# Kernel tuning notes

Measured on AMD Instinct MI355X. Metric: run time of the kernel, lower is better.

The kernel has to match this reference:

```python
import jax, jax.numpy as jnp
import numpy as np

K = 3  # dynamic filter kernel size
EPS = 1e-10


def _filter_norm_spatial(s, std_param):
    # s: (B, K*K, H, W); normalize over filter-tap dim (unbiased std, as torch)
    s = s - s.mean(axis=1, keepdims=True)
    s = s / (s.std(axis=1, keepdims=True, ddof=1) + EPS)
    return s * std_param[None, :, None, None]


def _filter_norm_channel(cf, std_param, B, C):
    # cf: (B, C*K*K); normalize over the K*K taps of each channel
    cf = cf.reshape(B, C, K * K)
    cf = cf - cf.mean(axis=2, keepdims=True)
    cf = cf / (cf.std(axis=2, keepdims=True, ddof=1) + EPS)
    cf = cf.reshape(B, C * K * K) * std_param[None, :]
    return cf.reshape(B, C, K * K)


def _ddf_pack(x, sw, sb, sstd, cw1, cb1, cw2, cb2, cstd):
    B, C, H, W = x.shape
    # spatial branch: 1x1 conv -> per-pixel K*K spatial filter
    s = jnp.einsum('bchw,oc->bohw', x, sw) + sb[None, :, None, None]
    s = _filter_norm_spatial(s, sstd)                      # (B, 9, H, W)
    # channel branch: GAP -> SE MLP -> per-channel K*K filter
    g = x.mean(axis=(2, 3))                                # (B, C)
    h = jax.nn.relu(g @ cw1.T + cb1)                       # (B, mid)
    cf = h @ cw2.T + cb2                                   # (B, C*9)
    cf = _filter_norm_channel(cf, cstd, B, C)              # (B, C, 9)
    # apply decoupled dynamic filter: w[b,c,uv,h,w] = cf[b,c,uv] * s[b,uv,h,w]
    pad = K // 2
    xp = jnp.pad(x, ((0, 0), (0, 0), (pad, pad), (pad, pad)))
    # patches: (B, C, 9, H, W) -- the 9 shifted views (unfold)
    patches = jnp.stack([xp[:, :, i:i + H, j:j + W]
                         for i in range(K) for j in range(K)], axis=2)
    return jnp.einsum('bckhw,bck,bkhw->bchw', patches, cf, s)


def setup_inputs() -> dict:
    key = jax.random.key(0)
    ks = jax.random.split(key, 20)
    nf, mid = 64, 12
    std_scale = np.sqrt(2.0) / K  # calculate_gain('relu') / kernel_size
    d = {'x': jax.random.normal(ks[0], (4, nf, 256, 256), jnp.float32)}
    i = 1
    for p in ('1', '2'):
        d['sw' + p] = jax.random.normal(ks[i], (K * K, nf), jnp.float32) * 0.1; i += 1
        d['sb' + p] = jax.random.normal(ks[i], (K * K,), jnp.float32) * 0.1; i += 1
        d['sstd' + p] = jax.random.normal(ks[i], (K * K,), jnp.float32) * std_scale; i += 1
        d['cw1_' + p] = jax.random.normal(ks[i], (mid, nf), jnp.float32) * 0.1; i += 1
        d['cb1_' + p] = jax.random.normal(ks[i], (mid,), jnp.float32) * 0.1; i += 1
        d['cw2_' + p] = jax.random.normal(ks[i], (nf * K * K, mid), jnp.float32) * 0.1; i += 1
        d['cb2_' + p] = jax.random.normal(ks[i], (nf * K * K,), jnp.float32) * 0.1; i += 1
        d['cstd' + p] = jax.random.normal(ks[i], (nf * K * K,), jnp.float32) * std_scale; i += 1
    return d


def reference(x, sw1, sb1, sstd1, cw1_1, cb1_1, cw2_1, cb2_1, cstd1,
              sw2, sb2, sstd2, cw1_2, cb1_2, cw2_2, cb2_2, cstd2):
    out = _ddf_pack(x, sw1, sb1, sstd1, cw1_1, cb1_1, cw2_1, cb2_1, cstd1)
    out = jax.nn.relu(out)
    out = _ddf_pack(out, sw2, sb2, sstd2, cw1_2, cb1_2, cw2_2, cb2_2, cstd2)
    return x + out
```

## Files before the change

### kernel.cpp

```cpp
#include <hip/hip_runtime.h>

#define B_ 4
#define C_ 64
#define H_ 256
#define W_ 256
#define HW_ (H_*W_)
#define MID_ 12
#define NPB_ 64

__device__ __forceinline__ float wave_reduce64(float v) {
#pragma unroll
    for (int off = 32; off; off >>= 1) v += __shfl_xor(v, off, 64);
    return v;
}

__global__ __launch_bounds__(256, 1) void prep_kernel(const float* __restrict__ x,
    const float* __restrict__ sw, const float* __restrict__ sb,
    const float* __restrict__ sstd, float* __restrict__ sarr, float* __restrict__ gp) {
    const int lane = threadIdx.x & 63, wv = threadIdx.x >> 6;
    const int row = blockIdx.x * 4 + wv;
    const int b = blockIdx.y;
    const int pix = row * W_ + lane * 4;
    __shared__ float lg[4][C_];

    float4 st[9];
#pragma unroll
    for (int t = 0; t < 9; ++t) { float v = sb[t]; st[t] = make_float4(v, v, v, v); }

    const float* xb = x + (size_t)b * C_ * HW_ + pix;
    float4 vA[4], vB[4];
#pragma unroll
    for (int i = 0; i < 4; ++i) vA[i] = *(const float4*)(xb + (size_t)i * HW_);

#define PREP_COMP(BUF, C0) do {                                               \
        _Pragma("unroll")                                                     \
        for (int i_ = 0; i_ < 4; ++i_) {                                      \
            const int c_ = (C0) + i_;                                         \
            float4 v_ = BUF[i_];                                              \
            _Pragma("unroll")                                                 \
            for (int t_ = 0; t_ < 9; ++t_) {                                  \
                const float wt_ = sw[t_ * C_ + c_];                           \
                st[t_].x = fmaf(v_.x, wt_, st[t_].x);                         \
                st[t_].y = fmaf(v_.y, wt_, st[t_].y);                         \
                st[t_].z = fmaf(v_.z, wt_, st[t_].z);                         \
                st[t_].w = fmaf(v_.w, wt_, st[t_].w);                         \
            }                                                                 \
            float g_ = wave_reduce64(((v_.x + v_.y) + (v_.z + v_.w)));        \
            if (lane == 0) lg[wv][c_] = g_;                                   \
        }                                                                     \
    } while (0)

    for (int k = 0; k < C_; k += 8) {
#pragma unroll
        for (int i = 0; i < 4; ++i) vB[i] = *(const float4*)(xb + (size_t)(k + 4 + i) * HW_);
        PREP_COMP(vA, k);
        if (k + 8 < C_) {
#pragma unroll
            for (int i = 0; i < 4; ++i) vA[i] = *(const float4*)(xb + (size_t)(k + 8 + i) * HW_);
        }
        PREP_COMP(vB, k + 4);
    }
#undef PREP_COMP

    {
        float4 mean = make_float4(0, 0, 0, 0);
#pragma unroll
        for (int t = 0; t < 9; ++t) {
            mean.x += st[t].x; mean.y += st[t].y; mean.z += st[t].z; mean.w += st[t].w;
        }
        mean.x *= (1.f/9.f); mean.y *= (1.f/9.f); mean.z *= (1.f/9.f); mean.w *= (1.f/9.f);
        float4 var = make_float4(0, 0, 0, 0);
#pragma unroll
        for (int t = 0; t < 9; ++t) {
            float dx = st[t].x - mean.x, dy = st[t].y - mean.y;
            float dz = st[t].z - mean.z, dw = st[t].w - mean.w;
            var.x = fmaf(dx, dx, var.x); var.y = fmaf(dy, dy, var.y);
            var.z = fmaf(dz, dz, var.z); var.w = fmaf(dw, dw, var.w);
        }
        float ix = 1.f / (sqrtf(var.x * (1.f/8.f)) + 1e-10f);
        float iy = 1.f / (sqrtf(var.y * (1.f/8.f)) + 1e-10f);
        float iz = 1.f / (sqrtf(var.z * (1.f/8.f)) + 1e-10f);
        float iw = 1.f / (sqrtf(var.w * (1.f/8.f)) + 1e-10f);
        float* sp = sarr + ((size_t)b * 9) * HW_ + pix;
#pragma unroll
        for (int t = 0; t < 9; ++t) {
            float sd = sstd[t];
            *(float4*)(sp + (size_t)t * HW_) = make_float4(
                (st[t].x - mean.x) * ix * sd, (st[t].y - mean.y) * iy * sd,
                (st[t].z - mean.z) * iz * sd, (st[t].w - mean.w) * iw * sd);
        }
    }
    __syncthreads();
    if (threadIdx.x < C_) {
        int c = threadIdx.x;
        float s4 = lg[0][c] + lg[1][c] + lg[2][c] + lg[3][c];
        gp[((size_t)b * C_ + c) * NPB_ + blockIdx.x] = s4;
    }
}

__global__ __launch_bounds__(256) void cfk(const float* __restrict__ gp,
    const float* __restrict__ cw1, const float* __restrict__ cb1,
    const float* __restrict__ cw2, const float* __restrict__ cb2,
    const float* __restrict__ cstd, float* __restrict__ cf) {
    const int tid = threadIdx.x;
    const int b = tid >> 6, c = tid & 63;
    __shared__ float gsm[B_][C_];
    __shared__ float hsm[B_][MID_];
    {
        const float4* p4 = (const float4*)(gp + ((size_t)b * C_ + c) * NPB_);
        float s = 0.f;
#pragma unroll
        for (int i = 0; i < NPB_ / 4; ++i) { float4 v = p4[i]; s += (v.x + v.y) + (v.z + v.w); }
        gsm[b][c] = s * (1.f / HW_);
    }
    __syncthreads();
    if (tid < B_ * MID_) {
        int b2 = tid / MID_, m = tid % MID_;
        float a = cb1[m];
        for (int cc = 0; cc < C_; ++cc) a = fmaf(gsm[b2][cc], cw1[m * C_ + cc], a);
        hsm[b2][m] = fmaxf(a, 0.f);
    }
    __syncthreads();
    float v[9];
    float mean = 0.f;
#pragma unroll
    for (int t = 0; t < 9; ++t) {
        int o = c * 9 + t;
        float a = cb2[o];
#pragma unroll
        for (int m = 0; m < MID_; ++m) a = fmaf(hsm[b][m], cw2[o * MID_ + m], a);
        v[t] = a;
        mean += a;
    }
    mean *= (1.f / 9.f);
    float var = 0.f;
#pragma unroll
    for (int t = 0; t < 9; ++t) { float d = v[t] - mean; var += d * d; }
    float inv = 1.f / (sqrtf(var * (1.f / 8.f)) + 1e-10f);
    float* o12 = cf + ((size_t)b * C_ + c) * 12;
#pragma unroll
    for (int t = 0; t < 9; ++t) o12[t] = (v[t] - mean) * inv * cstd[c * 9 + t];
    o12[9] = 0.f; o12[10] = 0.f; o12[11] = 0.f;
}

template<bool PASS1>
__global__ __launch_bounds__(256, 1) void apply_kernel(const float* __restrict__ in,
    const float* __restrict__ sarr, const float* __restrict__ cf,
    const float* __restrict__ swn, const float* __restrict__ sbn,
    const float* __restrict__ sstdn, const float* __restrict__ resid,
    float* __restrict__ out, float* __restrict__ snext, float* __restrict__ gpn) {
    const int lane = threadIdx.x & 63, wv = threadIdx.x >> 6;
    const int row = blockIdx.x * 4 + wv;
    const int b = blockIdx.y;
    const int c0 = PASS1 ? 0 : (blockIdx.z * 32);
    const int NCH = PASS1 ? 64 : 32;
    const int pix = row * W_ + lane * 4;
    __shared__ float lg[4][C_];

    const bool rup = row > 0, rdn = row < H_ - 1;
    const int offUp = rup ? -W_ : 0;
    const int offDn = rdn ? W_ : 0;
    const float fup = rup ? 1.f : 0.f;
    const float fdn = rdn ? 1.f : 0.f;

    float4 s0t[9];
    {
        const float* sp = sarr + ((size_t)b * 9) * HW_ + pix;
#pragma unroll
        for (int t = 0; t < 9; ++t) s0t[t] = *(const float4*)(sp + (size_t)t * HW_);
#pragma unroll
        for (int t = 0; t < 3; ++t) {
            s0t[t].x *= fup; s0t[t].y *= fup; s0t[t].z *= fup; s0t[t].w *= fup;
            s0t[t + 6].x *= fdn; s0t[t + 6].y *= fdn; s0t[t + 6].z *= fdn; s0t[t + 6].w *= fdn;
        }
        if (lane == 0)  { s0t[0].x = 0.f; s0t[3].x = 0.f; s0t[6].x = 0.f; }
        if (lane == 63) { s0t[2].w = 0.f; s0t[5].w = 0.f; s0t[8].w = 0.f; }
    }

    float4 nt[9];
    if (PASS1) {
#pragma unroll
        for (int t = 0; t < 9; ++t) { float v = sbn[t]; nt[t] = make_float4(v, v, v, v); }
    }

    const float* inb = in + (size_t)b * C_ * HW_ + pix;
    const float* cfb = cf + ((size_t)b * C_) * 12;
    const float* rb  = PASS1 ? nullptr : (resid + (size_t)b * C_ * HW_ + pix);
    float* outp = out + (size_t)b * C_ * HW_ + pix;

    float4 bufA[4][3], bufB[4][3], rA[4], rB[4];

#define LOADB(BUF, RV, CH0) do {                                              \
        _Pragma("unroll")                                                     \
        for (int i_ = 0; i_ < 4; ++i_) {                                      \
            const float* p_ = inb + (size_t)((CH0) + i_) * HW_;               \
            BUF[i_][0] = *(const float4*)(p_ + offUp);                        \
            BUF[i_][1] = *(const float4*)(p_);                                \
            BUF[i_][2] = *(const float4*)(p_ + offDn);                        \
            if (!PASS1) RV[i_] = *(const float4*)(rb + (size_t)((CH0) + i_) * HW_); \
        }                                                                     \
    } while (0)

#define COMPB(BUF, RV, CH0) do {                                              \
        _Pragma("unroll")                                                     \
        for (int i_ = 0; i_ < 4; ++i_) {                                      \
            const int ch_ = (CH0) + i_;                                       \
            const float* cfc_ = cfb + (size_t)ch_ * 12;                       \
            float4 acc_ = make_float4(0.f, 0.f, 0.f, 0.f);                    \
            _Pragma("unroll")                                                 \
            for (int dr_ = 0; dr_ < 3; ++dr_) {                               \
                float4 v_ = BUF[i_][dr_];                                     \
                float w0_ = __shfl_up(v_.w, 1, 64);                           \
                float w5_ = __shfl_down(v_.x, 1, 64);                         \
                const float w_[6] = {w0_, v_.x, v_.y, v_.z, v_.w, w5_};       \
                _Pragma("unroll")                                             \
                for (int dc_ = 0; dc_ < 3; ++dc_) {                           \
                    const int t_ = dr_ * 3 + dc_;                             \
                    const float cft_ = cfc_[t_];                              \
                    acc_.x = fmaf(w_[dc_ + 0] * s0t[t_].x, cft_, acc_.x);     \
                    acc_.y = fmaf(w_[dc_ + 1] * s0t[t_].y, cft_, acc_.y);     \
                    acc_.z = fmaf(w_[dc_ + 2] * s0t[t_].z, cft_, acc_.z);     \
                    acc_.w = fmaf(w_[dc_ + 3] * s0t[t_].w, cft_, acc_.w);     \
                }                                                             \
            }                                                                 \
            float4 o_;                                                        \
            if (PASS1) {                                                      \
                o_.x = fmaxf(acc_.x, 0.f); o_.y = fmaxf(acc_.y, 0.f);         \
                o_.z = fmaxf(acc_.z, 0.f); o_.w = fmaxf(acc_.w, 0.f);         \
                _Pragma("unroll")                                             \
                for (int t_ = 0; t_ < 9; ++t_) {                              \
                    const float wt_ = swn[t_ * C_ + ch_];                     \
                    nt[t_].x = fmaf(o_.x, wt_, nt[t_].x);                     \
                    nt[t_].y = fmaf(o_.y, wt_, nt[t_].y);                     \
                    nt[t_].z = fmaf(o_.z, wt_, nt[t_].z);                     \
                    nt[t_].w = fmaf(o_.w, wt_, nt[t_].w);                     \
                }                                                             \
                float g_ = wave_reduce64(((o_.x + o_.y) + (o_.z + o_.w)));    \
                if (lane == 0) lg[wv][ch_] = g_;                              \
            } else {                                                          \
                o_.x = acc_.x + RV[i_].x; o_.y = acc_.y + RV[i_].y;           \
                o_.z = acc_.z + RV[i_].z; o_.w = acc_.w + RV[i_].w;           \
            }                                                                 \
            *(float4*)(outp + (size_t)ch_ * HW_) = o_;                        \
        }                                                                     \
    } while (0)

    LOADB(bufA, rA, c0);
    for (int k = c0; k < c0 + NCH; k += 8) {
        LOADB(bufB, rB, k + 4);
        COMPB(bufA, rA, k);
        if (k + 8 < c0 + NCH) LOADB(bufA, rA, k + 8);
        COMPB(bufB, rB, k + 4);
    }
#undef LOADB
#undef COMPB

    if (PASS1) {
        float4 mean = make_float4(0, 0, 0, 0);
#pragma unroll
        for (int t = 0; t < 9; ++t) {
            mean.x += nt[t].x; mean.y += nt[t].y; mean.z += nt[t].z; mean.w += nt[t].w;
        }
        mean.x *= (1.f/9.f); mean.y *= (1.f/9.f); mean.z *= (1.f/9.f); mean.w *= (1.f/9.f);
        float4 var = make_float4(0, 0, 0, 0);
#pragma unroll
        for (int t = 0; t < 9; ++t) {
            float dx = nt[t].x - mean.x, dy = nt[t].y - mean.y;
            float dz = nt[t].z - mean.z, dw = nt[t].w - mean.w;
            var.x = fmaf(dx, dx, var.x); var.y = fmaf(dy, dy, var.y);
            var.z = fmaf(dz, dz, var.z); var.w = fmaf(dw, dw, var.w);
        }
        float ix = 1.f / (sqrtf(var.x * (1.f/8.f)) + 1e-10f);
        float iy = 1.f / (sqrtf(var.y * (1.f/8.f)) + 1e-10f);
        float iz = 1.f / (sqrtf(var.z * (1.f/8.f)) + 1e-10f);
        float iw = 1.f / (sqrtf(var.w * (1.f/8.f)) + 1e-10f);
        float* sp = snext + ((size_t)b * 9) * HW_ + pix;
#pragma unroll
        for (int t = 0; t < 9; ++t) {
            float sd = sstdn[t];
            *(float4*)(sp + (size_t)t * HW_) = make_float4(
                (nt[t].x - mean.x) * ix * sd, (nt[t].y - mean.y) * iy * sd,
                (nt[t].z - mean.z) * iz * sd, (nt[t].w - mean.w) * iw * sd);
        }
        __syncthreads();
        if (threadIdx.x < C_) {
            int c = threadIdx.x;
            float s4 = lg[0][c] + lg[1][c] + lg[2][c] + lg[3][c];
            gpn[((size_t)b * C_ + c) * NPB_ + blockIdx.x] = s4;
        }
    }
}

extern "C" void kernel_launch(void* const* d_in, const int* in_sizes, int n_in,
                              void* d_out, int out_size, void* d_ws, size_t ws_size,
                              hipStream_t stream) {
    const float* x     = (const float*)d_in[0];
    const float* sw1   = (const float*)d_in[1];
    const float* sb1   = (const float*)d_in[2];
    const float* sstd1 = (const float*)d_in[3];
    const float* cw1_1 = (const float*)d_in[4];
    const float* cb1_1 = (const float*)d_in[5];
    const float* cw2_1 = (const float*)d_in[6];
    const float* cb2_1 = (const float*)d_in[7];
    const float* cstd1 = (const float*)d_in[8];
    const float* sw2   = (const float*)d_in[9];
    const float* sb2   = (const float*)d_in[10];
    const float* sstd2 = (const float*)d_in[11];
    const float* cw1_2 = (const float*)d_in[12];
    const float* cb1_2 = (const float*)d_in[13];
    const float* cw2_2 = (const float*)d_in[14];
    const float* cb2_2 = (const float*)d_in[15];
    const float* cstd2 = (const float*)d_in[16];
    float* outp = (float*)d_out;

    const size_t n_out1 = (size_t)B_ * C_ * HW_;
    const size_t n_s    = (size_t)B_ * 9 * HW_;
    const size_t n_cf   = (size_t)B_ * C_ * 12;
    const size_t n_gp   = (size_t)B_ * C_ * NPB_;
    const size_t need = (n_out1 + 2 * n_s + 2 * n_cf + 2 * n_gp) * sizeof(float);
    if (ws_size < need) return;

    float* out1 = (float*)d_ws;
    float* s1   = out1 + n_out1;
    float* s2   = s1 + n_s;
    float* cf1  = s2 + n_s;
    float* cf2  = cf1 + n_cf;
    float* gp1  = cf2 + n_cf;
    float* gp2  = gp1 + n_gp;

    dim3 g1(H_ / 4, B_);
    dim3 g2(H_ / 4, B_, 2);

    prep_kernel<<<g1, 256, 0, stream>>>(x, sw1, sb1, sstd1, s1, gp1);
    cfk<<<1, 256, 0, stream>>>(gp1, cw1_1, cb1_1, cw2_1, cb2_1, cstd1, cf1);
    apply_kernel<true><<<g1, 256, 0, stream>>>(x, s1, cf1, sw2, sb2, sstd2,
                                               nullptr, out1, s2, gp2);
    cfk<<<1, 256, 0, stream>>>(gp2, cw1_2, cb1_2, cw2_2, cb2_2, cstd2, cf2);
    apply_kernel<false><<<g2, 256, 0, stream>>>(out1, s2, cf2, nullptr, nullptr,
                                                nullptr, x, outp, nullptr, nullptr);
}
```

Before: 151.3 us.

## Split channels across waves per row and reduce spatial partials through LDS

Prep and apply kernels now process one image row per block, with each of the four waves handling a 16-channel slice instead of its own row. The per-wave partial spatial-filter sums are combined through shared memory by wave 0, which then normalizes and stores them. Pooling partials are written straight to global memory, with four times as many per-channel slots. Launch bounds are raised so more blocks fit per CU, and the apply kernel remaps row order across blocks. This adds parallelism and occupancy, at the cost of an LDS reduction, a barrier, wave 0 doing the normalization alone, and a larger cfk reduction.

```diff
diff --git a/kernel.cpp b/kernel.cpp
--- a/kernel.cpp
+++ b/kernel.cpp
@@ -6,7 +6,7 @@
 #define W_ 256
 #define HW_ (H_*W_)
 #define MID_ 12
-#define NPB_ 64
+#define NPB_ 256
 
 __device__ __forceinline__ float wave_reduce64(float v) {
 #pragma unroll
@@ -14,28 +14,58 @@
     return v;
 }
 
-__global__ __launch_bounds__(256, 1) void prep_kernel(const float* __restrict__ x,
+__device__ __forceinline__ void fnorm4_store(const float4* t9,
+    const float* __restrict__ sstd, float* sp) {
+    float4 mean = make_float4(0, 0, 0, 0);
+#pragma unroll
+    for (int t = 0; t < 9; ++t) {
+        mean.x += t9[t].x; mean.y += t9[t].y; mean.z += t9[t].z; mean.w += t9[t].w;
+    }
+    mean.x *= (1.f/9.f); mean.y *= (1.f/9.f); mean.z *= (1.f/9.f); mean.w *= (1.f/9.f);
+    float4 var = make_float4(0, 0, 0, 0);
+#pragma unroll
+    for (int t = 0; t < 9; ++t) {
+        float dx = t9[t].x - mean.x, dy = t9[t].y - mean.y;
+        float dz = t9[t].z - mean.z, dw = t9[t].w - mean.w;
+        var.x = fmaf(dx, dx, var.x); var.y = fmaf(dy, dy, var.y);
+        var.z = fmaf(dz, dz, var.z); var.w = fmaf(dw, dw, var.w);
+    }
+    float ix = 1.f / (sqrtf(var.x * (1.f/8.f)) + 1e-10f);
+    float iy = 1.f / (sqrtf(var.y * (1.f/8.f)) + 1e-10f);
+    float iz = 1.f / (sqrtf(var.z * (1.f/8.f)) + 1e-10f);
+    float iw = 1.f / (sqrtf(var.w * (1.f/8.f)) + 1e-10f);
+#pragma unroll
+    for (int t = 0; t < 9; ++t) {
+        float sd = sstd[t];
+        *(float4*)(sp + (size_t)t * HW_) = make_float4(
+            (t9[t].x - mean.x) * ix * sd, (t9[t].y - mean.y) * iy * sd,
+            (t9[t].z - mean.z) * iz * sd, (t9[t].w - mean.w) * iw * sd);
+    }
+}
+
+__global__ __launch_bounds__(256, 4) void prep_kernel(const float* __restrict__ x,
     const float* __restrict__ sw, const float* __restrict__ sb,
     const float* __restrict__ sstd, float* __restrict__ sarr, float* __restrict__ gp) {
     const int lane = threadIdx.x & 63, wv = threadIdx.x >> 6;
-    const int row = blockIdx.x * 4 + wv;
+    const int row = blockIdx.x;
     const int b = blockIdx.y;
+    const int c0 = wv * 16;
     const int pix = row * W_ + lane * 4;
-    __shared__ float lg[4][C_];
+    __shared__ float4 stl[3][9][64];
 
     float4 st[9];
 #pragma unroll
-    for (int t = 0; t < 9; ++t) { float v = sb[t]; st[t] = make_float4(v, v, v, v); }
+    for (int t = 0; t < 9; ++t) st[t] = make_float4(0, 0, 0, 0);
 
     const float* xb = x + (size_t)b * C_ * HW_ + pix;
     float4 vA[4], vB[4];
 #pragma unroll
-    for (int i = 0; i < 4; ++i) vA[i] = *(const float4*)(xb + (size_t)i * HW_);
-
-#define PREP_COMP(BUF, C0) do {                                               \
+    for (int i = 0; i < 4; ++i) vA[i] = *(const float4*)(xb + (size_t)(c0 + i) * HW_);
+
+#define PREP_COMP(BUF, CC) do {                                               \
         _Pragma("unroll")                                                     \
         for (int i_ = 0; i_ < 4; ++i_) {                                      \
-            const int c_ = (C0) + i_;                                         \
+            const int c_ = (CC) + i_;                                         \
             float4 v_ = BUF[i_];                                              \
             _Pragma("unroll")                                                 \
             for (int t_ = 0; t_ < 9; ++t_) {                                  \
@@ -46,55 +76,39 @@
                 st[t_].w = fmaf(v_.w, wt_, st[t_].w);                         \
             }                                                                 \
             float g_ = wave_reduce64(((v_.x + v_.y) + (v_.z + v_.w)));        \
-            if (lane == 0) lg[wv][c_] = g_;                                   \
+            if (lane == 0) gp[((size_t)b * C_ + c_) * NPB_ + blockIdx.x] = g_; \
         }                                                                     \
     } while (0)
 
-    for (int k = 0; k < C_; k += 8) {
-#pragma unroll
-        for (int i = 0; i < 4; ++i) vB[i] = *(const float4*)(xb + (size_t)(k + 4 + i) * HW_);
-        PREP_COMP(vA, k);
-        if (k + 8 < C_) {
-#pragma unroll
-            for (int i = 0; i < 4; ++i) vA[i] = *(const float4*)(xb + (size_t)(k + 8 + i) * HW_);
-        }
-        PREP_COMP(vB, k + 4);
+    for (int k = 0; k < 16; k += 8) {
+#pragma unroll
+        for (int i = 0; i < 4; ++i) vB[i] = *(const float4*)(xb + (size_t)(c0 + k + 4 + i) * HW_);
+        PREP_COMP(vA, c0 + k);
+        if (k + 8 < 16) {
+#pragma unroll
+            for (int i = 0; i < 4; ++i) vA[i] = *(const float4*)(xb + (size_t)(c0 + k + 8 + i) * HW_);
+        }
+        PREP_COMP(vB, c0 + k + 4);
     }
 #undef PREP_COMP
 
-    {
-        float4 mean = make_float4(0, 0, 0, 0);
+    if (wv) {
+#pragma unroll
+        for (int t = 0; t < 9; ++t) stl[wv - 1][t][lane] = st[t];
+    }
+    __syncthreads();
+    if (wv == 0) {
 #pragma unroll
         for (int t = 0; t < 9; ++t) {
-            mean.x += st[t].x; mean.y += st[t].y; mean.z += st[t].z; mean.w += st[t].w;
-        }
-        mean.x *= (1.f/9.f); mean.y *= (1.f/9.f); mean.z *= (1.f/9.f); mean.w *= (1.f/9.f);
-        float4 var = make_float4(0, 0, 0, 0);
-#pragma unroll
-        for (int t = 0; t < 9; ++t) {
-            float dx = st[t].x - mean.x, dy = st[t].y - mean.y;
-            float dz = st[t].z - mean.z, dw = st[t].w - mean.w;
-            var.x = fmaf(dx, dx, var.x); var.y = fmaf(dy, dy, var.y);
-            var.z = fmaf(dz, dz, var.z); var.w = fmaf(dw, dw, var.w);
-        }
-        float ix = 1.f / (sqrtf(var.x * (1.f/8.f)) + 1e-10f);
-        float iy = 1.f / (sqrtf(var.y * (1.f/8.f)) + 1e-10f);
-        float iz = 1.f / (sqrtf(var.z * (1.f/8.f)) + 1e-10f);
-        float iw = 1.f / (sqrtf(var.w * (1.f/8.f)) + 1e-10f);
-        float* sp = sarr + ((size_t)b * 9) * HW_ + pix;
-#pragma unroll
-        for (int t = 0; t < 9; ++t) {
-            float sd = sstd[t];
-            *(float4*)(sp + (size_t)t * HW_) = make_float4(
-                (st[t].x - mean.x) * ix * sd, (st[t].y - mean.y) * iy * sd,
-                (st[t].z - mean.z) * iz * sd, (st[t].w - mean.w) * iw * sd);
-        }
-    }
-    __syncthreads();
-    if (threadIdx.x < C_) {
-        int c = threadIdx.x;
-        float s4 = lg[0][c] + lg[1][c] + lg[2][c] + lg[3][c];
-        gp[((size_t)b * C_ + c) * NPB_ + blockIdx.x] = s4;
+            float bb = sb[t];
+#pragma unroll
+            for (int j = 0; j < 3; ++j) {
+                float4 o = stl[j][t][lane];
+                st[t].x += o.x; st[t].y += o.y; st[t].z += o.z; st[t].w += o.w;
+            }
+            st[t].x += bb; st[t].y += bb; st[t].z += bb; st[t].w += bb;
+        }
+        fnorm4_store(st, sstd, sarr + ((size_t)b * 9) * HW_ + pix);
     }
 }
 
@@ -109,7 +123,7 @@
     {
         const float4* p4 = (const float4*)(gp + ((size_t)b * C_ + c) * NPB_);
         float s = 0.f;
-#pragma unroll
+#pragma unroll 8
         for (int i = 0; i < NPB_ / 4; ++i) { float4 v = p4[i]; s += (v.x + v.y) + (v.z + v.w); }
         gsm[b][c] = s * (1.f / HW_);
     }
@@ -143,19 +157,18 @@
     o12[9] = 0.f; o12[10] = 0.f; o12[11] = 0.f;
 }
 
-template<bool PASS1>
-__global__ __launch_bounds__(256, 1) void apply_kernel(const float* __restrict__ in,
+template<bool PASS1, int MINW>
+__global__ __launch_bounds__(256, MINW) void apply_kernel(const float* __restrict__ in,
     const float* __restrict__ sarr, const float* __restrict__ cf,
     const float* __restrict__ swn, const float* __restrict__ sbn,
     const float* __restrict__ sstdn, const float* __restrict__ resid,
     float* __restrict__ out, float* __restrict__ snext, float* __restrict__ gpn) {
     const int lane = threadIdx.x & 63, wv = threadIdx.x >> 6;
-    const int row = blockIdx.x * 4 + wv;
+    const int f = blockIdx.x;
+    const int row = ((f & 7) << 5) | (f >> 3);
     const int b = blockIdx.y;
-    const int c0 = PASS1 ? 0 : (blockIdx.z * 32);
-    const int NCH = PASS1 ? 64 : 32;
+    const int c0 = wv * 16;
     const int pix = row * W_ + lane * 4;
-    __shared__ float lg[4][C_];
 
     const bool rup = row > 0, rdn = row < H_ - 1;
     const int offUp = rup ? -W_ : 0;
@@ -180,7 +193,7 @@
     float4 nt[9];
     if (PASS1) {
 #pragma unroll
-        for (int t = 0; t < 9; ++t) { float v = sbn[t]; nt[t] = make_float4(v, v, v, v); }
+        for (int t = 0; t < 9; ++t) nt[t] = make_float4(0, 0, 0, 0);
     }
 
     const float* inb = in + (size_t)b * C_ * HW_ + pix;
@@ -188,11 +201,11 @@
     const float* rb  = PASS1 ? nullptr : (resid + (size_t)b * C_ * HW_ + pix);
     float* outp = out + (size_t)b * C_ * HW_ + pix;
 
-    float4 bufA[4][3], bufB[4][3], rA[4], rB[4];
+    float4 bufA[2][3], bufB[2][3], rA[2], rB[2];
 
 #define LOADB(BUF, RV, CH0) do {                                              \
         _Pragma("unroll")                                                     \
-        for (int i_ = 0; i_ < 4; ++i_) {                                      \
+        for (int i_ = 0; i_ < 2; ++i_) {                                      \
             const float* p_ = inb + (size_t)((CH0) + i_) * HW_;               \
             BUF[i_][0] = *(const float4*)(p_ + offUp);                        \
             BUF[i_][1] = *(const float4*)(p_);                                \
@@ -203,7 +216,7 @@
 
 #define COMPB(BUF, RV, CH0) do {                                              \
         _Pragma("unroll")                                                     \
-        for (int i_ = 0; i_ < 4; ++i_) {                                      \
+        for (int i_ = 0; i_ < 2; ++i_) {                                      \
             const int ch_ = (CH0) + i_;                                       \
             const float* cfc_ = cfb + (size_t)ch_ * 12;                       \
             float4 acc_ = make_float4(0.f, 0.f, 0.f, 0.f);                    \
@@ -236,7 +249,7 @@
                     nt[t_].w = fmaf(o_.w, wt_, nt[t_].w);                     \
                 }                                                             \
                 float g_ = wave_reduce64(((o_.x + o_.y) + (o_.z + o_.w)));    \
-                if (lane == 0) lg[wv][ch_] = g_;                              \
+                if (lane == 0) gpn[((size_t)b * C_ + ch_) * NPB_ + f] = g_;   \
             } else {                                                          \
                 o_.x = acc_.x + RV[i_].x; o_.y = acc_.y + RV[i_].y;           \
                 o_.z = acc_.z + RV[i_].z; o_.w = acc_.w + RV[i_].w;           \
@@ -246,47 +259,35 @@
     } while (0)
 
     LOADB(bufA, rA, c0);
-    for (int k = c0; k < c0 + NCH; k += 8) {
-        LOADB(bufB, rB, k + 4);
-        COMPB(bufA, rA, k);
-        if (k + 8 < c0 + NCH) LOADB(bufA, rA, k + 8);
-        COMPB(bufB, rB, k + 4);
+#pragma unroll
+    for (int k = 0; k < 16; k += 4) {
+        LOADB(bufB, rB, c0 + k + 2);
+        COMPB(bufA, rA, c0 + k);
+        if (k + 4 < 16) LOADB(bufA, rA, c0 + k + 4);
+        COMPB(bufB, rB, c0 + k + 2);
     }
 #undef LOADB
 #undef COMPB
 
-    if (PASS1) {
-        float4 mean = make_float4(0, 0, 0, 0);
-#pragma unroll
-        for (int t = 0; t < 9; ++t) {
-            mean.x += nt[t].x; mean.y += nt[t].y; mean.z += nt[t].z; mean.w += nt[t].w;
-        }
-        mean.x *= (1.f/9.f); mean.y *= (1.f/9.f); mean.z *= (1.f/9.f); mean.w *= (1.f/9.f);
-        float4 var = make_float4(0, 0, 0, 0);
-#pragma unroll
-        for (int t = 0; t < 9; ++t) {
-            float dx = nt[t].x - mean.x, dy = nt[t].y - mean.y;
-            float dz = nt[t].z - mean.z, dw = nt[t].w - mean.w;
-            var.x = fmaf(dx, dx, var.x); var.y = fmaf(dy, dy, var.y);
-            var.z = fmaf(dz, dz, var.z); var.w = fmaf(dw, dw, var.w);
-        }
-        float ix = 1.f / (sqrtf(var.x * (1.f/8.f)) + 1e-10f);
-        float iy = 1.f / (sqrtf(var.y * (1.f/8.f)) + 1e-10f);
-        float iz = 1.f / (sqrtf(var.z * (1.f/8.f)) + 1e-10f);
-        float iw = 1.f / (sqrtf(var.w * (1.f/8.f)) + 1e-10f);
-        float* sp = snext + ((size_t)b * 9) * HW_ + pix;
-#pragma unroll
-        for (int t = 0; t < 9; ++t) {
-            float sd = sstdn[t];
-            *(float4*)(sp + (size_t)t * HW_) = make_float4(
-                (nt[t].x - mean.x) * ix * sd, (nt[t].y - mean.y) * iy * sd,
-                (nt[t].z - mean.z) * iz * sd, (nt[t].w - mean.w) * iw * sd);
+    if constexpr (PASS1) {
+        __shared__ float4 ntl[3][9][64];
+        if (wv) {
+#pragma unroll
+            for (int t = 0; t < 9; ++t) ntl[wv - 1][t][lane] = nt[t];
         }
         __syncthreads();
-        if (threadIdx.x < C_) {
-            int c = threadIdx.x;
-            float s4 = lg[0][c] + lg[1][c] + lg[2][c] + lg[3][c];
-            gpn[((size_t)b * C_ + c) * NPB_ + blockIdx.x] = s4;
+        if (wv == 0) {
+#pragma unroll
+            for (int t = 0; t < 9; ++t) {
+                float bb = sbn[t];
+#pragma unroll
+                for (int j = 0; j < 3; ++j) {
+                    float4 o = ntl[j][t][lane];
+                    nt[t].x += o.x; nt[t].y += o.y; nt[t].z += o.z; nt[t].w += o.w;
+                }
+                nt[t].x += bb; nt[t].y += bb; nt[t].z += bb; nt[t].w += bb;
+            }
+            fnorm4_store(nt, sstdn, snext + ((size_t)b * 9) * HW_ + pix);
         }
     }
 }
@@ -328,14 +329,13 @@
     float* gp1  = cf2 + n_cf;
     float* gp2  = gp1 + n_gp;
 
-    dim3 g1(H_ / 4, B_);
-    dim3 g2(H_ / 4, B_, 2);
-
-    prep_kernel<<<g1, 256, 0, stream>>>(x, sw1, sb1, sstd1, s1, gp1);
+    dim3 g(H_, B_);
+
+    prep_kernel<<<g, 256, 0, stream>>>(x, sw1, sb1, sstd1, s1, gp1);
     cfk<<<1, 256, 0, stream>>>(gp1, cw1_1, cb1_1, cw2_1, cb2_1, cstd1, cf1);
-    apply_kernel<true><<<g1, 256, 0, stream>>>(x, s1, cf1, sw2, sb2, sstd2,
-                                               nullptr, out1, s2, gp2);
+    apply_kernel<true, 3><<<g, 256, 0, stream>>>(x, s1, cf1, sw2, sb2, sstd2,
+                                                 nullptr, out1, s2, gp2);
     cfk<<<1, 256, 0, stream>>>(gp2, cw1_2, cb1_2, cw2_2, cb2_2, cstd2, cf2);
-    apply_kernel<false><<<g2, 256, 0, stream>>>(out1, s2, cf2, nullptr, nullptr,
-                                                nullptr, x, outp, nullptr, nullptr);
-}
+    apply_kernel<false, 4><<<g, 256, 0, stream>>>(out1, s2, cf2, nullptr, nullptr,
+                                                  nullptr, x, outp, nullptr, nullptr);
+}
```

Measured after the change: 392.4 us. 2.59x slower.
